# Kernel tuning notes

Hardware: AMD Instinct MI355X
Metric: run time of the kernel (lower is better)

The kernel has to match this reference:

```python
import jax, jax.numpy as jnp
import numpy as np

B, T, C = 256, 168, 1024
N_SEQ = 168
HORIZON = 24


def setup_inputs() -> dict:
    key = jax.random.key(0)
    k1, k2, k3, k4 = jax.random.split(key, 4)
    x = jax.random.normal(k1, (B, T, C), dtype=jnp.float32)
    y = jax.random.normal(k2, (B, T, C), dtype=jnp.float32)
    # nn.Linear(n_seq, 1): weight [1, n_seq], bias [1]
    w = jax.random.normal(k3, (1, N_SEQ), dtype=jnp.float32) / jnp.sqrt(jnp.float32(N_SEQ))
    b = jax.random.normal(k4, (1,), dtype=jnp.float32) * 0.01
    return {"x": x, "y": y, "w": w, "b": b}


def reference(x, y, w, b):
    # x is unused in the original torch forward.
    n_seq = w.shape[1]
    yt = jnp.transpose(y, (0, 2, 1))          # [B, C, T]
    buf0 = yt[:, :, -n_seq:]                  # rolling window [B, C, n_seq]
    wv = w[0]                                 # [n_seq]
    bv = b[0]

    def step(buf, _):
        pred = jnp.einsum('bcn,n->bc', buf, wv) + bv   # [B, C]
        buf = jnp.concatenate([buf[:, :, 1:], pred[:, :, None]], axis=2)
        return buf, pred

    _, preds = jax.lax.scan(step, buf0, None, length=HORIZON)  # [H, B, C]
    # equivalent to y[:, :, -horizon:].permute(0, 2, 1) -> [B, H, C]
    return jnp.transpose(preds, (1, 0, 2))
```

## Files before the change

### kernel.cpp

```cpp
#include <hip/hip_runtime.h>

#define B_ 256
#define T_ 168
#define C_ 1024
#define H_ 24
#define TH 84


__global__ __launch_bounds__(192) void ar_precompute(const float* __restrict__ w,
                                                     const float* __restrict__ bias,
                                                     float* __restrict__ ws) {
    __shared__ float lw[T_];
    const int t = threadIdx.x;
    if (t < T_) lw[t] = w[t];
    __syncthreads();
    if (t < T_) {
        float col[H_];
        #pragma unroll
        for (int k = 0; k < H_; ++k) {
            float v = (t >= k) ? lw[t - k] : 0.0f;
            #pragma unroll
            for (int j = 0; j < k; ++j)
                v += lw[T_ - k + j] * col[j];
            col[k] = v;
        }
        #pragma unroll
        for (int k = 0; k < H_; ++k)
            ws[t * H_ + k] = col[k];
    } else if (t == T_) {
        float bv = bias[0];
        float beta[H_];
        #pragma unroll
        for (int k = 0; k < H_; ++k) {
            float v = bv;
            #pragma unroll
            for (int j = 0; j < k; ++j)
                v += lw[T_ - k + j] * beta[j];
            beta[k] = v;
        }
        #pragma unroll
        for (int k = 0; k < H_; ++k)
            ws[T_ * H_ + k] = beta[k];
    }
}

__global__ __launch_bounds__(256, 8) void ar_main(const float* __restrict__ y,
                                                  const float* __restrict__ ws,
                                                  float* __restrict__ out) {
    __shared__ float sacc[H_ * 128];

    const int tid = threadIdx.x;
    const int c_local = tid & 127;
    const int h = __builtin_amdgcn_readfirstlane(tid >> 7);

    const int c = blockIdx.x * 128 + c_local;
    const int b = blockIdx.y;
    const float* __restrict__ yp =
        y + (size_t)b * (size_t)(T_ * C_) + (size_t)(h * TH) * C_ + c;

    float acc[H_];
    #pragma unroll
    for (int k = 0; k < H_; ++k) acc[k] = 0.0f;

    #pragma unroll 4
    for (int tt = 0; tt < TH; ++tt) {
        const float yv = yp[(size_t)tt * C_];
        const float4* __restrict__ w4 = (const float4*)(ws + (h * TH + tt) * H_);
        #pragma unroll
        for (int q = 0; q < H_ / 4; ++q) {
            const float4 wv = w4[q];
            acc[4 * q + 0] += wv.x * yv;
            acc[4 * q + 1] += wv.y * yv;
            acc[4 * q + 2] += wv.z * yv;
            acc[4 * q + 3] += wv.w * yv;
        }
    }

    if (h == 1) {
        #pragma unroll
        for (int k = 0; k < H_; ++k)
            sacc[k * 128 + c_local] = acc[k];
    }
    __syncthreads();
    if (h == 0) {
        const float* __restrict__ beta = ws + T_ * H_;
        float* __restrict__ op = out + ((size_t)b * H_) * C_ + c;
        #pragma unroll
        for (int k = 0; k < H_; ++k)
            op[(size_t)k * C_] = acc[k] + sacc[k * 128 + c_local] + beta[k];
    }
}

extern "C" void kernel_launch(void* const* d_in, const int* in_sizes, int n_in,
                              void* d_out, int out_size, void* d_ws, size_t ws_size,
                              hipStream_t stream) {
    const float* y    = (const float*)d_in[1];
    const float* w    = (const float*)d_in[2];
    const float* bias = (const float*)d_in[3];
    float* out = (float*)d_out;
    float* ws  = (float*)d_ws;

    ar_precompute<<<1, 192, 0, stream>>>(w, bias, ws);
    ar_main<<<dim3(C_ / 128, B_), 256, 0, stream>>>(y, ws, out);
}
```

Baseline: 40.85 us.

## Fuse AR precompute into main kernel using sliding weight window and in-kernel recurrence

```diff
diff --git a/kernel.cpp b/kernel.cpp
--- a/kernel.cpp
+++ b/kernel.cpp
@@ -5,48 +5,12 @@
 #define C_ 1024
 #define H_ 24
 #define TH 84
+#define WW 28
 
-
-__global__ __launch_bounds__(192) void ar_precompute(const float* __restrict__ w,
-                                                     const float* __restrict__ bias,
-                                                     float* __restrict__ ws) {
-    __shared__ float lw[T_];
-    const int t = threadIdx.x;
-    if (t < T_) lw[t] = w[t];
-    __syncthreads();
-    if (t < T_) {
-        float col[H_];
-        #pragma unroll
-        for (int k = 0; k < H_; ++k) {
-            float v = (t >= k) ? lw[t - k] : 0.0f;
-            #pragma unroll
-            for (int j = 0; j < k; ++j)
-                v += lw[T_ - k + j] * col[j];
-            col[k] = v;
-        }
-        #pragma unroll
-        for (int k = 0; k < H_; ++k)
-            ws[t * H_ + k] = col[k];
-    } else if (t == T_) {
-        float bv = bias[0];
-        float beta[H_];
-        #pragma unroll
-        for (int k = 0; k < H_; ++k) {
-            float v = bv;
-            #pragma unroll
-            for (int j = 0; j < k; ++j)
-                v += lw[T_ - k + j] * beta[j];
-            beta[k] = v;
-        }
-        #pragma unroll
-        for (int k = 0; k < H_; ++k)
-            ws[T_ * H_ + k] = beta[k];
-    }
-}
-
-__global__ __launch_bounds__(256, 8) void ar_main(const float* __restrict__ y,
-                                                  const float* __restrict__ ws,
-                                                  float* __restrict__ out) {
+__global__ __launch_bounds__(256, 8) void ar_fused(const float* __restrict__ y,
+                                                   const float* __restrict__ w,
+                                                   const float* __restrict__ bias,
+                                                   float* __restrict__ out) {
     __shared__ float sacc[H_ * 128];
 
     const int tid = threadIdx.x;
@@ -62,17 +26,22 @@
     #pragma unroll
     for (int k = 0; k < H_; ++k) acc[k] = 0.0f;
 
-    #pragma unroll 4
-    for (int tt = 0; tt < TH; ++tt) {
-        const float yv = yp[(size_t)tt * C_];
-        const float4* __restrict__ w4 = (const float4*)(ws + (h * TH + tt) * H_);
+    float win[WW];
+    #pragma unroll
+    for (int s = 0; s < WW; ++s) win[s] = 0.0f;
+    if (h == 1) {
         #pragma unroll
-        for (int q = 0; q < H_ / 4; ++q) {
-            const float4 wv = w4[q];
-            acc[4 * q + 0] += wv.x * yv;
-            acc[4 * q + 1] += wv.y * yv;
-            acc[4 * q + 2] += wv.z * yv;
-            acc[4 * q + 3] += wv.w * yv;
+        for (int d = 1; d <= H_ - 1; ++d) win[WW - d] = w[TH - d];
+    }
+
+    for (int tb = 0; tb < TH / WW; ++tb) {
+        #pragma unroll
+        for (int j = 0; j < WW; ++j) {
+            win[j] = w[h * TH + tb * WW + j];
+            const float yv = yp[(size_t)(tb * WW + j) * C_];
+            #pragma unroll
+            for (int k = 0; k < H_; ++k)
+                acc[k] += win[(j - k + WW) % WW] * yv;
         }
     }
 
@@ -83,11 +52,21 @@
     }
     __syncthreads();
     if (h == 0) {
-        const float* __restrict__ beta = ws + T_ * H_;
+        float wtail[H_ - 1];
+        #pragma unroll
+        for (int i = 0; i < H_ - 1; ++i) wtail[i] = w[T_ - (H_ - 1) + i];
+        const float bv = bias[0];
+        float pred[H_];
         float* __restrict__ op = out + ((size_t)b * H_) * C_ + c;
         #pragma unroll
-        for (int k = 0; k < H_; ++k)
-            op[(size_t)k * C_] = acc[k] + sacc[k * 128 + c_local] + beta[k];
+        for (int k = 0; k < H_; ++k) {
+            float v = acc[k] + sacc[k * 128 + c_local] + bv;
+            #pragma unroll
+            for (int j = 0; j < k; ++j)
+                v += wtail[H_ - 1 - k + j] * pred[j];
+            pred[k] = v;
+            op[(size_t)k * C_] = v;
+        }
     }
 }
 
@@ -98,8 +77,6 @@
     const float* w    = (const float*)d_in[2];
     const float* bias = (const float*)d_in[3];
     float* out = (float*)d_out;
-    float* ws  = (float*)d_ws;
 
-    ar_precompute<<<1, 192, 0, stream>>>(w, bias, ws);
-    ar_main<<<dim3(C_ / 128, B_), 256, 0, stream>>>(y, ws, out);
+    ar_fused<<<dim3(C_ / 128, B_), 256, 0, stream>>>(y, w, bias, out);
 }
```

Result: slower. 45.70 us (+11.9%).
